# Kernel tuning notes

Hardware: AMD Instinct MI355X
Metric: run time of the kernel (lower is better)

Reference implementation:

```python
import jax, jax.numpy as jnp
import numpy as np

B, T = 1048576, 8
ALPHA = 1.1
COMMISSION = 0.05
BET_PCT = 0.02  # assumed bet_percentage (undefined in original __init__)
TAU = 0.1
EPS = 1e-8


def setup_inputs() -> dict:
    key = jax.random.key(0)
    k1, k2, k3, k4 = jax.random.split(key, 4)
    # network outputs are probabilities (used as probs in entropy/profit terms)
    predicted_probs = jax.nn.softmax(jax.random.normal(k1, (B, T), dtype=jnp.float32), axis=1)
    # one-hot true winners
    winner_idx = jax.random.randint(k2, (B,), 0, T)
    true_winners = jax.nn.one_hot(winner_idx, T, dtype=jnp.float32)
    # decimal odds in [1.5, 15): valid and complete field for nearly all races
    market_odds = jax.random.uniform(k3, (B, T), dtype=jnp.float32, minval=1.5, maxval=15.0)
    # explicit Gumbel(0,1) noise standing in for F.gumbel_softmax's internal sample
    u = jax.random.uniform(k4, (B, T), dtype=jnp.float32, minval=1e-6, maxval=1.0 - 1e-6)
    gumbel_noise = -jnp.log(-jnp.log(u))
    return {"predicted_probs": predicted_probs, "true_winners": true_winners,
            "market_odds": market_odds, "gumbel_noise": gumbel_noise}


def reference(predicted_probs, true_winners, market_odds, gumbel_noise):
    batch_size = predicted_probs.shape[0]
    # race validity
    has_valid_odds = jnp.any(market_odds > 0, axis=1)
    implied_probs = 1.0 / jnp.clip(market_odds, 1.01)
    has_complete_field = implied_probs.sum(axis=1) >= 0.95
    valid = has_valid_odds & has_complete_field  # [B]

    # masked expected profit per dog
    ep = jnp.where(valid[:, None],
                   (market_odds * ALPHA * predicted_probs - 1.0) * BET_PCT * (1.0 - COMMISSION),
                   0.0)  # [B,T]

    # gumbel-softmax selection (logits = ep / temperature, tau = temperature)
    soft_selection = jax.nn.softmax((ep / TAU + gumbel_noise) / TAU, axis=1)
    soft_expected_profits = (soft_selection * ep).sum(axis=1)  # [B]

    # prediction cross-entropy (probs treated as logits, per original code)
    labels = jnp.argmax(true_winners, axis=1)
    logp = jax.nn.log_softmax(predicted_probs, axis=1)
    ce = -jnp.take_along_axis(logp, labels[:, None], axis=1)[:, 0]  # [B]

    valid_f = valid.astype(ce.dtype)
    cnt = valid_f.sum()
    prediction_loss = jnp.where(cnt > 0, (ce * valid_f).sum() / jnp.maximum(cnt, 1.0), ce.mean())

    confidence_penalty = -predicted_probs.max(axis=1).mean() * 0.1
    betting_loss = jnp.where(cnt > 0, -(soft_expected_profits * valid_f).sum() / batch_size,
                             confidence_penalty)

    entropy_reg = -(predicted_probs * jnp.log(predicted_probs + EPS)).sum(axis=1).mean()

    lambda_betting = jnp.minimum(0.5 + cnt / 10000.0 * 0.5, 1.0)
    lambda_entropy = 0.01
    loss = prediction_loss + lambda_betting * betting_loss - lambda_entropy * entropy_reg
    return loss
```

## Files before the change

kernel.cpp:

```cpp
#include <hip/hip_runtime.h>
#include <math.h>


constexpr int T = 8;
constexpr int NB = 1024;
constexpr int NT = 256;

__device__ __forceinline__ float fastrcp(float x) {
  return __builtin_amdgcn_rcpf(x);
}

__global__ __launch_bounds__(NT, 4) void betting_main(
    const float4* __restrict__ pp4, const float4* __restrict__ tw4,
    const float4* __restrict__ mo4, const float4* __restrict__ gn4,
    float* __restrict__ partials, int nraces) {
  const int tid = blockIdx.x * NT + threadIdx.x;
  const int ntot = gridDim.x * NT;

  float acc[6] = {0.f, 0.f, 0.f, 0.f, 0.f, 0.f};

  for (int r = tid; r < nraces; r += ntot) {
    float4 a0 = pp4[2 * r], a1 = pp4[2 * r + 1];
    float4 b0 = tw4[2 * r], b1 = tw4[2 * r + 1];
    float4 c0 = mo4[2 * r], c1 = mo4[2 * r + 1];
    float4 d0 = gn4[2 * r], d1 = gn4[2 * r + 1];
    __builtin_amdgcn_sched_barrier(0);

    float p[T] = {a0.x, a0.y, a0.z, a0.w, a1.x, a1.y, a1.z, a1.w};
    float w[T] = {b0.x, b0.y, b0.z, b0.w, b1.x, b1.y, b1.z, b1.w};
    float o[T] = {c0.x, c0.y, c0.z, c0.w, c1.x, c1.y, c1.z, c1.w};
    float g[T] = {d0.x, d0.y, d0.z, d0.w, d1.x, d1.y, d1.z, d1.w};

    bool anypos = false;
    float simp = 0.f;
#pragma unroll
    for (int t = 0; t < T; ++t) {
      anypos = anypos || (o[t] > 0.f);
      simp += fastrcp(fmaxf(o[t], 1.01f));
    }
    float vf = (anypos && simp >= 0.95f) ? 1.f : 0.f;

    float ep[T];
#pragma unroll
    for (int t = 0; t < T; ++t)
      ep[t] = (o[t] * 1.1f * p[t] - 1.f) * (0.02f * 0.95f) * vf;

    float z[T], zm = -INFINITY;
#pragma unroll
    for (int t = 0; t < T; ++t) {
      z[t] = ep[t] * 100.f + g[t] * 10.f;
      zm = fmaxf(zm, z[t]);
    }
    float s2 = 0.f, sp = 0.f;
#pragma unroll
    for (int t = 0; t < T; ++t) {
      float e = __expf(z[t] - zm);
      s2 += e;
      sp += e * ep[t];
    }
    float soft_ep = sp * fastrcp(s2);

    float m = -INFINITY;
#pragma unroll
    for (int t = 0; t < T; ++t) m = fmaxf(m, p[t]);
    float se = 0.f, pl = 0.f;
#pragma unroll
    for (int t = 0; t < T; ++t) {
      se += __expf(p[t] - m);
      pl += w[t] * p[t];
    }
    float ce = m + __logf(se) - pl;

    float ent = 0.f;
#pragma unroll
    for (int t = 0; t < T; ++t) ent -= p[t] * __logf(p[t] + 1e-8f);

    acc[0] += vf;
    acc[1] += ce * vf;
    acc[2] += ce;
    acc[3] += soft_ep * vf;
    acc[4] += m;
    acc[5] += ent;
  }

  __shared__ float red[NT / 64][6];
#pragma unroll
  for (int k = 0; k < 6; ++k) {
#pragma unroll
    for (int off = 32; off >= 1; off >>= 1) acc[k] += __shfl_down(acc[k], off);
  }
  int lane = threadIdx.x & 63, wave = threadIdx.x >> 6;
  if (lane == 0) {
#pragma unroll
    for (int k = 0; k < 6; ++k) red[wave][k] = acc[k];
  }
  __syncthreads();
  if (threadIdx.x == 0) {
#pragma unroll
    for (int k = 0; k < 6; ++k) {
      float s = red[0][k] + red[1][k] + red[2][k] + red[3][k];
      partials[k * gridDim.x + blockIdx.x] = s;
    }
  }
}

__global__ __launch_bounds__(NT) void betting_final(
    const float* __restrict__ partials, int nb, float* __restrict__ out,
    double Bd) {
  __shared__ double red[NT / 64][6];
  double a[6] = {0, 0, 0, 0, 0, 0};
#pragma unroll
  for (int k = 0; k < 6; ++k)
    for (int i = threadIdx.x; i < nb; i += NT) a[k] += (double)partials[k * nb + i];
#pragma unroll
  for (int k = 0; k < 6; ++k) {
#pragma unroll
    for (int off = 32; off >= 1; off >>= 1) a[k] += __shfl_down(a[k], off);
  }
  int lane = threadIdx.x & 63, wave = threadIdx.x >> 6;
  if (lane == 0) {
#pragma unroll
    for (int k = 0; k < 6; ++k) red[wave][k] = a[k];
  }
  __syncthreads();
  if (threadIdx.x == 0) {
    double s[6];
#pragma unroll
    for (int k = 0; k < 6; ++k)
      s[k] = red[0][k] + red[1][k] + red[2][k] + red[3][k];
    double cnt = s[0], Scev = s[1], Sce = s[2], Ssoft = s[3], Smax = s[4],
           Sent = s[5];
    double pred = (cnt > 0.0) ? Scev / fmax(cnt, 1.0) : Sce / Bd;
    double conf = -(Smax / Bd) * 0.1;
    double bet = (cnt > 0.0) ? -Ssoft / Bd : conf;
    double entr = Sent / Bd;
    double lam = fmin(0.5 + cnt / 10000.0 * 0.5, 1.0);
    out[0] = (float)(pred + lam * bet - 0.01 * entr);
  }
}

extern "C" void kernel_launch(void* const* d_in, const int* in_sizes, int n_in,
                              void* d_out, int out_size, void* d_ws,
                              size_t ws_size, hipStream_t stream) {
  const float4* pp = (const float4*)d_in[0];
  const float4* tw = (const float4*)d_in[1];
  const float4* mo = (const float4*)d_in[2];
  const float4* gn = (const float4*)d_in[3];
  float* out = (float*)d_out;
  float* partials = (float*)d_ws;

  const int nraces = in_sizes[0] / T;

  int nb = NB;
  while ((size_t)(6 * nb * 4) > ws_size && nb > 64) nb >>= 1;

  betting_main<<<nb, NT, 0, stream>>>(pp, tw, mo, gn, partials, nraces);
  betting_final<<<1, NT, 0, stream>>>(partials, nb, out, (double)nraces);
}
```

Measured before the change: 35.53 us.

## Stage inputs via global_load_lds double buffering with half-race-per-lane compute

Adds a fast path that asynchronously copies input chunks from global memory into per-wave LDS double buffers using global_load_lds, overlapping the next chunk's loads with compute on the current one. Each lane now handles half a race (4 teams), and partner lanes combine max/sum terms through xor shuffles. Each block covers a fixed 1024 races, so the grid is sized from the input (1024 blocks here) instead of a fixed grid-stride loop. The fast path only applies when the race count divides evenly; otherwise the old generic kernel is used. The risks are extra LDS round-trips and shuffle overhead on what is a memory-bound stream.

```diff
diff --git a/kernel.cpp b/kernel.cpp
--- a/kernel.cpp
+++ b/kernel.cpp
@@ -1,16 +1,157 @@
 #include <hip/hip_runtime.h>
 #include <math.h>
+#include <stdint.h>
 
 
 constexpr int T = 8;
-constexpr int NB = 1024;
 constexpr int NT = 256;
+constexpr int WAVES = NT / 64;
+constexpr int RACES_PER_BLOCK = 1024;
+constexpr int RACES_PER_WAVE = RACES_PER_BLOCK / WAVES;
+constexpr int CHUNK_RACES = 32;
+constexpr int NCHUNK = RACES_PER_WAVE / CHUNK_RACES;
+constexpr int CHUNK_B = CHUNK_RACES * 32;
+
+typedef const __attribute__((address_space(1))) void gas_t;
+typedef __attribute__((address_space(3))) void las_t;
 
 __device__ __forceinline__ float fastrcp(float x) {
   return __builtin_amdgcn_rcpf(x);
 }
 
-__global__ __launch_bounds__(NT, 4) void betting_main(
+__device__ __forceinline__ void block_reduce_publish(
+    float acc[6], float* __restrict__ partials) {
+  __shared__ float red[WAVES][6];
+#pragma unroll
+  for (int k = 0; k < 6; ++k) {
+#pragma unroll
+    for (int off = 32; off >= 1; off >>= 1) acc[k] += __shfl_down(acc[k], off);
+  }
+  const int lane = threadIdx.x & 63, wave = threadIdx.x >> 6;
+  if (lane == 0) {
+#pragma unroll
+    for (int k = 0; k < 6; ++k) red[wave][k] = acc[k];
+  }
+  __syncthreads();
+  if (threadIdx.x == 0) {
+#pragma unroll
+    for (int k = 0; k < 6; ++k) {
+      float s = red[0][k] + red[1][k] + red[2][k] + red[3][k];
+      partials[k * gridDim.x + blockIdx.x] = s;
+    }
+  }
+}
+
+__global__ __launch_bounds__(NT, 4) void betting_lds(
+    const char* __restrict__ pp, const char* __restrict__ tw,
+    const char* __restrict__ mo, const char* __restrict__ gn,
+    float* __restrict__ partials) {
+  __shared__ uint8_t stg[WAVES][2][4][CHUNK_B];
+  const int wave = threadIdx.x >> 6, lane = threadIdx.x & 63;
+
+  const long base0 =
+      ((long)blockIdx.x * RACES_PER_BLOCK + (long)wave * RACES_PER_WAVE) * 32;
+  const char* ga0 = pp + base0;
+  const char* ga1 = tw + base0;
+  const char* ga2 = mo + base0;
+  const char* ga3 = gn + base0;
+
+  float acc[6] = {0.f, 0.f, 0.f, 0.f, 0.f, 0.f};
+
+  auto stage = [&](int j, int buf) {
+    const long off = (long)j * CHUNK_B + (long)lane * 16;
+    __builtin_amdgcn_global_load_lds((gas_t*)(ga0 + off),
+                                     (las_t*)&stg[wave][buf][0][0], 16, 0, 0);
+    __builtin_amdgcn_global_load_lds((gas_t*)(ga1 + off),
+                                     (las_t*)&stg[wave][buf][1][0], 16, 0, 0);
+    __builtin_amdgcn_global_load_lds((gas_t*)(ga2 + off),
+                                     (las_t*)&stg[wave][buf][2][0], 16, 0, 0);
+    __builtin_amdgcn_global_load_lds((gas_t*)(ga3 + off),
+                                     (las_t*)&stg[wave][buf][3][0], 16, 0, 0);
+  };
+
+  auto consume = [&](int buf) {
+    const int lb = lane * 16;
+    float4 av = *(const float4*)&stg[wave][buf][0][lb];
+    float4 wv = *(const float4*)&stg[wave][buf][1][lb];
+    float4 ov = *(const float4*)&stg[wave][buf][2][lb];
+    float4 gv = *(const float4*)&stg[wave][buf][3][lb];
+    float p[4] = {av.x, av.y, av.z, av.w};
+    float w[4] = {wv.x, wv.y, wv.z, wv.w};
+    float o[4] = {ov.x, ov.y, ov.z, ov.w};
+    float g[4] = {gv.x, gv.y, gv.z, gv.w};
+
+    float anyp = 0.f, simp = 0.f;
+#pragma unroll
+    for (int t = 0; t < 4; ++t) {
+      anyp = fmaxf(anyp, (o[t] > 0.f) ? 1.f : 0.f);
+      simp += fastrcp(fmaxf(o[t], 1.01f));
+    }
+    anyp = fmaxf(anyp, __shfl_xor(anyp, 1));
+    simp = simp + __shfl_xor(simp, 1);
+    float vf = (anyp > 0.5f && simp >= 0.95f) ? 1.f : 0.f;
+
+    float ep[4];
+#pragma unroll
+    for (int t = 0; t < 4; ++t)
+      ep[t] = (o[t] * 1.1f * p[t] - 1.f) * (0.02f * 0.95f) * vf;
+
+    float z[4], zmh = -INFINITY;
+#pragma unroll
+    for (int t = 0; t < 4; ++t) {
+      z[t] = ep[t] * 100.f + g[t] * 10.f;
+      zmh = fmaxf(zmh, z[t]);
+    }
+    float zm = fmaxf(zmh, __shfl_xor(zmh, 1));
+    float s2h = 0.f, sph = 0.f;
+#pragma unroll
+    for (int t = 0; t < 4; ++t) {
+      float e = __expf(z[t] - zm);
+      s2h += e;
+      sph += e * ep[t];
+    }
+    float s2 = s2h + __shfl_xor(s2h, 1);
+    float sp = sph + __shfl_xor(sph, 1);
+    float soft_ep = sp * fastrcp(s2);
+
+    float mh = fmaxf(fmaxf(p[0], p[1]), fmaxf(p[2], p[3]));
+    float m = fmaxf(mh, __shfl_xor(mh, 1));
+    float seh = 0.f, plh = 0.f;
+#pragma unroll
+    for (int t = 0; t < 4; ++t) {
+      seh += __expf(p[t] - m);
+      plh += w[t] * p[t];
+    }
+    float se = seh + __shfl_xor(seh, 1);
+    float celin = 0.5f * (m + __logf(se)) - plh;
+
+    float enth = 0.f;
+#pragma unroll
+    for (int t = 0; t < 4; ++t) enth -= p[t] * __logf(p[t] + 1e-8f);
+
+    acc[0] += 0.5f * vf;
+    acc[1] += celin * vf;
+    acc[2] += celin;
+    acc[3] += 0.5f * soft_ep * vf;
+    acc[4] += 0.5f * m;
+    acc[5] += enth;
+  };
+
+  stage(0, 0);
+  for (int j = 0; j < NCHUNK - 1; ++j) {
+    stage(j + 1, (j + 1) & 1);
+    asm volatile("s_waitcnt vmcnt(4)" ::: "memory");
+    __builtin_amdgcn_sched_barrier(0);
+    consume(j & 1);
+  }
+  asm volatile("s_waitcnt vmcnt(0)" ::: "memory");
+  __builtin_amdgcn_sched_barrier(0);
+  consume((NCHUNK - 1) & 1);
+
+  block_reduce_publish(acc, partials);
+}
+
+__global__ __launch_bounds__(NT, 4) void betting_generic(
     const float4* __restrict__ pp4, const float4* __restrict__ tw4,
     const float4* __restrict__ mo4, const float4* __restrict__ gn4,
     float* __restrict__ partials, int nraces) {
@@ -18,14 +159,11 @@
   const int ntot = gridDim.x * NT;
 
   float acc[6] = {0.f, 0.f, 0.f, 0.f, 0.f, 0.f};
-
   for (int r = tid; r < nraces; r += ntot) {
     float4 a0 = pp4[2 * r], a1 = pp4[2 * r + 1];
     float4 b0 = tw4[2 * r], b1 = tw4[2 * r + 1];
     float4 c0 = mo4[2 * r], c1 = mo4[2 * r + 1];
     float4 d0 = gn4[2 * r], d1 = gn4[2 * r + 1];
-    __builtin_amdgcn_sched_barrier(0);
-
     float p[T] = {a0.x, a0.y, a0.z, a0.w, a1.x, a1.y, a1.z, a1.w};
     float w[T] = {b0.x, b0.y, b0.z, b0.w, b1.x, b1.y, b1.z, b1.w};
     float o[T] = {c0.x, c0.y, c0.z, c0.w, c1.x, c1.y, c1.z, c1.w};
@@ -82,26 +220,7 @@
     acc[4] += m;
     acc[5] += ent;
   }
-
-  __shared__ float red[NT / 64][6];
-#pragma unroll
-  for (int k = 0; k < 6; ++k) {
-#pragma unroll
-    for (int off = 32; off >= 1; off >>= 1) acc[k] += __shfl_down(acc[k], off);
-  }
-  int lane = threadIdx.x & 63, wave = threadIdx.x >> 6;
-  if (lane == 0) {
-#pragma unroll
-    for (int k = 0; k < 6; ++k) red[wave][k] = acc[k];
-  }
-  __syncthreads();
-  if (threadIdx.x == 0) {
-#pragma unroll
-    for (int k = 0; k < 6; ++k) {
-      float s = red[0][k] + red[1][k] + red[2][k] + red[3][k];
-      partials[k * gridDim.x + blockIdx.x] = s;
-    }
-  }
+  block_reduce_publish(acc, partials);
 }
 
 __global__ __launch_bounds__(NT) void betting_final(
@@ -142,18 +261,27 @@
 extern "C" void kernel_launch(void* const* d_in, const int* in_sizes, int n_in,
                               void* d_out, int out_size, void* d_ws,
                               size_t ws_size, hipStream_t stream) {
-  const float4* pp = (const float4*)d_in[0];
-  const float4* tw = (const float4*)d_in[1];
-  const float4* mo = (const float4*)d_in[2];
-  const float4* gn = (const float4*)d_in[3];
+  const char* pp = (const char*)d_in[0];
+  const char* tw = (const char*)d_in[1];
+  const char* mo = (const char*)d_in[2];
+  const char* gn = (const char*)d_in[3];
   float* out = (float*)d_out;
   float* partials = (float*)d_ws;
 
   const int nraces = in_sizes[0] / T;
 
-  int nb = NB;
-  while ((size_t)(6 * nb * 4) > ws_size && nb > 64) nb >>= 1;
-
-  betting_main<<<nb, NT, 0, stream>>>(pp, tw, mo, gn, partials, nraces);
-  betting_final<<<1, NT, 0, stream>>>(partials, nb, out, (double)nraces);
-}
+  if (nraces > 0 && nraces % RACES_PER_BLOCK == 0 &&
+      (size_t)(6 * (nraces / RACES_PER_BLOCK) * 4) <= ws_size &&
+      nraces / RACES_PER_BLOCK <= 65535) {
+    const int nb = nraces / RACES_PER_BLOCK;
+    betting_lds<<<nb, NT, 0, stream>>>(pp, tw, mo, gn, partials);
+    betting_final<<<1, NT, 0, stream>>>(partials, nb, out, (double)nraces);
+  } else {
+    int nb = 1024;
+    while ((size_t)(6 * nb * 4) > ws_size && nb > 64) nb >>= 1;
+    betting_generic<<<nb, NT, 0, stream>>>(
+        (const float4*)pp, (const float4*)tw, (const float4*)mo,
+        (const float4*)gn, partials, nraces);
+    betting_final<<<1, NT, 0, stream>>>(partials, nb, out, (double)nraces);
+  }
+}
```

Measured after the change: 36.39 us. +2.4%, slower.
